# Kernel tuning notes

Measured on AMD Instinct MI355X. Metric: run time of the kernel, lower is better.

The kernel has to match this reference:

```python
import jax, jax.numpy as jnp
import numpy as np

D_MODEL = 1024
D_STATE = 32
EXPAND = 2
D_INNER = D_MODEL * EXPAND
B_SZ = 2
SEQ = 512


def setup_inputs() -> dict:
    key = jax.random.key(0)
    ks = jax.random.split(key, 10)
    x = jax.random.normal(ks[0], (B_SZ, SEQ, D_MODEL), dtype=jnp.float32)
    W_in = jax.random.normal(ks[1], (2 * D_INNER, D_MODEL), dtype=jnp.float32) * 0.02
    A_log = jax.random.uniform(ks[2], (D_INNER, D_STATE), minval=-4.0, maxval=-1.0, dtype=jnp.float32)
    W_B = jax.random.normal(ks[3], (D_STATE, D_MODEL), dtype=jnp.float32) * 0.02
    W_C = jax.random.normal(ks[4], (D_STATE, D_MODEL), dtype=jnp.float32) * 0.02
    W_dt = jax.random.normal(ks[5], (D_INNER, D_MODEL), dtype=jnp.float32) * 0.02
    b_dt = jnp.zeros((D_INNER,), dtype=jnp.float32)
    dt_bias = jnp.zeros((D_INNER,), dtype=jnp.float32) - 4.0
    rope_freq = jax.random.normal(ks[6], (D_STATE // 2,), dtype=jnp.float32) * 0.01
    ln_w = jnp.ones((D_INNER,), dtype=jnp.float32)
    ln_b = jnp.zeros((D_INNER,), dtype=jnp.float32)
    W_out = jax.random.normal(ks[7], (D_MODEL, D_INNER), dtype=jnp.float32) * 0.02
    return {"x": x, "W_in": W_in, "A_log": A_log, "W_B": W_B, "W_C": W_C,
            "W_dt": W_dt, "b_dt": b_dt, "dt_bias": dt_bias, "rope_freq": rope_freq,
            "ln_w": ln_w, "ln_b": ln_b, "W_out": W_out}


def _forward(x, W_in, A_log, W_B, W_C, W_dt, b_dt, dt_bias, rope_freq, ln_w, ln_b, W_out):
    B, L, _ = x.shape
    half = D_STATE // 2
    offset = 0

    xz = jnp.einsum('bld,ed->ble', x, W_in)                 # [B,L,2*D_INNER]
    x_inner = xz[..., :D_INNER]                             # [B,L,DI]
    z = jax.nn.silu(xz[..., D_INNER:])                      # [B,L,DI]

    A = -jnp.exp(A_log)                                     # [DI,DS]
    Bm = jnp.einsum('bld,nd->bln', x, W_B)                  # [B,L,DS]
    Cm = jnp.einsum('bld,nd->bln', x, W_C)                  # [B,L,DS]
    dt = jax.nn.softplus(jnp.einsum('bld,ed->ble', x, W_dt) + b_dt + dt_bias)  # [B,L,DI]

    # trapezoidal discretization
    dtA = dt[..., None] * A                                 # [B,L,DI,DS]
    denom = 1.0 - dtA / 2.0
    A_bar = (1.0 + dtA / 2.0) / denom                       # [B,L,DI,DS]
    B_bar = dt[..., None] / denom                           # [B,L,DI,DS]

    # per-step rope rotation angles: angle_t = rope_freq * (t + offset)
    t_idx = jnp.arange(L, dtype=jnp.float32) + offset       # [L]
    ang = t_idx[:, None] * rope_freq                        # [L,half]
    cos_a = jnp.cos(ang)
    sin_a = jnp.sin(ang)

    def step(state, inp):
        A_t, Bb_t, B_t, x_t, C_t, c_t, s_t = inp
        # state update: [B,DI,DS]
        state = A_t * state + Bb_t * B_t[:, None, :] * x_t[:, :, None]
        real = state[..., :half]
        imag = state[..., half:]
        state = jnp.concatenate([real * c_t - imag * s_t,
                                 real * s_t + imag * c_t], axis=-1)
        y_t = jnp.einsum('bds,bs->bd', state, C_t)          # [B,DI]
        return state, y_t

    state0 = jnp.zeros((B, D_INNER, D_STATE), dtype=x.dtype)
    xs = (jnp.swapaxes(A_bar, 0, 1), jnp.swapaxes(B_bar, 0, 1),
          jnp.swapaxes(Bm, 0, 1), jnp.swapaxes(x_inner, 0, 1),
          jnp.swapaxes(Cm, 0, 1), cos_a, sin_a)
    final_state, ys = jax.lax.scan(step, state0, xs)        # ys: [L,B,DI]
    out = jnp.swapaxes(ys, 0, 1) * z                        # [B,L,DI]

    # LayerNorm over last dim (eps=1e-5, torch default)
    mu = jnp.mean(out, axis=-1, keepdims=True)
    var = jnp.mean((out - mu) ** 2, axis=-1, keepdims=True)
    out = (out - mu) * jax.lax.rsqrt(var + 1e-5) * ln_w + ln_b

    out = jnp.einsum('ble,de->bld', out, W_out)             # [B,L,D_MODEL]
    return out, final_state


def reference(x, W_in, A_log, W_B, W_C, W_dt, b_dt, dt_bias, rope_freq, ln_w, ln_b, W_out):
    return _forward(x, W_in, A_log, W_B, W_C, W_dt, b_dt, dt_bias, rope_freq, ln_w, ln_b, W_out)
```

## Files before the change

### kernel.cpp

```cpp
#include <hip/hip_runtime.h>
#include <math.h>

#define B_SZ 2
#define SEQ 512
#define DM 1024
#define DI 2048
#define DS 32
#define TOK (B_SZ*SEQ)
#define NCH 8
#define CLEN (SEQ/NCH)
#define NPAIRH 32768

#define NFUSED 6272

typedef float v2f __attribute__((ext_vector_type(2)));

__device__ __forceinline__ unsigned short f2bf(float f) {
  unsigned int u = __builtin_bit_cast(unsigned int, f);
  unsigned int r = u + 0x7fffu + ((u >> 16) & 1u);
  return (unsigned short)(r >> 16);
}

template<int CTRL>
__device__ __forceinline__ float row_ror_add(float x) {
  int s = __builtin_amdgcn_update_dpp(0, __builtin_bit_cast(int, x), CTRL, 0xf, 0xf, false);
  return x + __builtin_bit_cast(float, s);
}
__device__ __forceinline__ float row16_sum(float v) {
  v = row_ror_add<0x121>(v);
  v = row_ror_add<0x122>(v);
  v = row_ror_add<0x124>(v);
  v = row_ror_add<0x128>(v);
  return v;
}

__global__ __launch_bounds__(256) void fused_cast(const float* __restrict__ x,
                                                  const float* __restrict__ W_in,
                                                  const float* __restrict__ W_dt,
                                                  const float* __restrict__ W_B,
                                                  const float* __restrict__ W_C,
                                                  const float* __restrict__ W_out,
                                                  unsigned short* __restrict__ xb,
                                                  unsigned short* __restrict__ wcat,
                                                  unsigned short* __restrict__ wob) {
  int g = blockIdx.x * 256 + threadIdx.x;
  const float* s; unsigned short* dd; int off;
  if      (g <  131072) { s = x;     dd = xb;             off = 0; }
  else if (g <  655360) { s = W_in;  dd = wcat;           off = 131072; }
  else if (g <  917504) { s = W_dt;  dd = wcat + 4194304; off = 655360; }
  else if (g <  921600) { s = W_B;   dd = wcat + 6291456; off = 917504; }
  else if (g <  925696) { s = W_C;   dd = wcat + 6324224; off = 921600; }
  else if (g < 1187840) { s = W_out; dd = wob;            off = 925696; }
  else return;
  int i = g - off;
  float4 a = ((const float4*)s)[i * 2];
  float4 b = ((const float4*)s)[i * 2 + 1];
  union { unsigned short us[8]; uint4 v; } o;
  o.us[0] = f2bf(a.x); o.us[1] = f2bf(a.y); o.us[2] = f2bf(a.z); o.us[3] = f2bf(a.w);
  o.us[4] = f2bf(b.x); o.us[5] = f2bf(b.y); o.us[6] = f2bf(b.z); o.us[7] = f2bf(b.w);
  ((uint4*)dd)[i] = o.v;
}

typedef __attribute__((ext_vector_type(8))) short  frag8;
typedef __attribute__((ext_vector_type(4))) float  facc4;

__device__ __forceinline__ void gload_lds16(const unsigned short* g, unsigned short* l) {
  __builtin_amdgcn_global_load_lds((const __attribute__((address_space(1))) unsigned int*)g,
                                   (__attribute__((address_space(3))) unsigned int*)l, 16, 0, 0);
}
__device__ __forceinline__ void gload_lds16f(const float* g, float* l) {
  __builtin_amdgcn_global_load_lds((const __attribute__((address_space(1))) unsigned int*)g,
                                   (__attribute__((address_space(3))) unsigned int*)l, 16, 0, 0);
}

__device__ __forceinline__ float softplus_fast(float v) {
  return fmaxf(v, 0.f) + __logf(1.f + __expf(-fabsf(v)));
}

template<int BMt, int BNt, int MT, bool ROUTE>
__global__ __launch_bounds__(256) void gemm_mfma(const unsigned short* __restrict__ A,
                                                 const unsigned short* __restrict__ Bw,
                                                 int K,
                                                 float* __restrict__ o_xs,
                                                 float* __restrict__ o_zb,
                                                 float* __restrict__ o_dts,
                                                 float* __restrict__ o_bcb,
                                                 const float* __restrict__ b_dt,
                                                 const float* __restrict__ dt_bias,
                                                 float* __restrict__ o_c, int ldc) {
  constexpr int FM = BMt / 32, FN = BNt / 32;
  constexpr int IA = BMt / 64, IB = BNt / 64;
  __shared__ __align__(16) unsigned short As[BMt * 32];
  __shared__ __align__(16) unsigned short Bs[BNt * 32];
  const int tid = threadIdx.x;
  const int w = tid >> 6, lane = tid & 63;
  const int wm = w >> 1, wn = w & 1;
  const int bid = blockIdx.x;
  const int Wk = (bid & 7) * ((int)gridDim.x >> 3) + (bid >> 3);
  const int m0 = (Wk % MT) * BMt;
  const int n0 = (Wk / MT) * BNt;
  const int r = lane & 15, q = lane >> 4;
  const int grow = lane >> 2, gk = (lane & 3) * 8;
  facc4 acc[FM][FN] = {};
  const unsigned short* Ag = A + (size_t)m0 * K + gk;
  const unsigned short* Bg = Bw + (size_t)n0 * K + gk;

  for (int k0 = 0; k0 < K; k0 += 32) {
#pragma unroll
    for (int i = 0; i < IA; ++i) {
      int ch = i * 4 + w;
      gload_lds16(Ag + (size_t)(ch * 16 + grow) * K + k0, &As[ch * 512]);
    }
#pragma unroll
    for (int i = 0; i < IB; ++i) {
      int ch = i * 4 + w;
      gload_lds16(Bg + (size_t)(ch * 16 + grow) * K + k0, &Bs[ch * 512]);
    }
    __syncthreads();
    frag8 af[FM], bf[FN];
#pragma unroll
    for (int i = 0; i < FM; ++i)
      af[i] = *(const frag8*)&As[(wm * (BMt / 2) + i * 16 + r) * 32 + q * 8];
#pragma unroll
    for (int jj = 0; jj < FN; ++jj)
      bf[jj] = *(const frag8*)&Bs[(wn * (BNt / 2) + jj * 16 + r) * 32 + q * 8];
#pragma unroll
    for (int i = 0; i < FM; ++i)
#pragma unroll
      for (int jj = 0; jj < FN; ++jj)
        acc[i][jj] = __builtin_amdgcn_mfma_f32_16x16x32_bf16(af[i], bf[jj], acc[i][jj], 0, 0, 0);
    __syncthreads();
  }

#pragma unroll
  for (int i = 0; i < FM; ++i) {
#pragma unroll
    for (int jj = 0; jj < FN; ++jj) {
      int n = n0 + wn * (BNt / 2) + jj * 16 + r;
      int mb = m0 + wm * (BMt / 2) + i * 16 + q * 4;
      if (ROUTE) {
        if (n < 2048) {
#pragma unroll
          for (int rg = 0; rg < 4; ++rg)
            o_xs[(size_t)(mb + rg) * DI + n] = acc[i][jj][rg];
        } else if (n < 4096) {
#pragma unroll
          for (int rg = 0; rg < 4; ++rg)
            o_zb[(size_t)(mb + rg) * DI + (n - 2048)] = acc[i][jj][rg];
        } else if (n < 6144) {
          int d = n - 4096;
          float bias = b_dt[d] + dt_bias[d];
#pragma unroll
          for (int rg = 0; rg < 4; ++rg)
            o_dts[(size_t)(mb + rg) * DI + d] = softplus_fast(acc[i][jj][rg] + bias);
        } else if (n < 6176) {
#pragma unroll
          for (int rg = 0; rg < 4; ++rg)
            o_bcb[(size_t)(mb + rg) * DS + (n - 6144)] = acc[i][jj][rg];
        } else if (n < 6208) {
#pragma unroll
          for (int rg = 0; rg < 4; ++rg)
            o_bcb[(size_t)TOK * DS + (size_t)(mb + rg) * DS + (n - 6176)] = acc[i][jj][rg];
        }
      } else {
#pragma unroll
        for (int rg = 0; rg < 4; ++rg)
          o_c[(size_t)(mb + rg) * ldc + n] = acc[i][jj][rg];
      }
    }
  }
}


__global__ __launch_bounds__(256) void scan_p1(const float* __restrict__ xs,
                                               const float* __restrict__ dts,
                                               const float* __restrict__ bcb,
                                               const float* __restrict__ A_log,
                                               const float* __restrict__ rope,
                                               float* __restrict__ Pbuf) {
  __shared__ __align__(16) float lds[6144];
  const int blk = blockIdx.x;
  const int c = blk >> 7;
  const int sub = blk & 127;
  const int b = sub >> 6;
  const int dbase = (sub & 63) << 5;
  const int tid = threadIdx.x;
  const int wv = tid >> 6, lane = tid & 63;
  const int j = tid & 15;
  const int ca = (tid >> 4) & 15;
  const int l0 = c * CLEN;
  const size_t base = (size_t)(b * SEQ + l0);

  {
    int row = wv * 16 + (lane >> 3);
    int col = (lane & 7) << 2;
#pragma unroll
    for (int k = 0; k < 2; ++k) {
      gload_lds16f(xs  + (base + row + k * 8) * DI + dbase + col, &lds[(wv * 16 + k * 8) * 32]);
      gload_lds16f(dts + (base + row + k * 8) * DI + dbase + col, &lds[2048 + (wv * 16 + k * 8) * 32]);
    }
#pragma unroll
    for (int k = 0; k < 2; ++k) {
      int seg = wv * 2 + k;
      gload_lds16f(bcb + base * DS + seg * 256 + lane * 4, &lds[4096 + seg * 256]);
    }
  }

  const int dA = dbase + 2 * ca;
  v2f Ar, Ai;
  Ar.x = -0.5f * expf(A_log[dA * DS + j]);
  Ar.y = -0.5f * expf(A_log[(dA + 1) * DS + j]);
  Ai.x = -0.5f * expf(A_log[dA * DS + j + 16]);
  Ai.y = -0.5f * expf(A_log[(dA + 1) * DS + j + 16]);
  const float fr = rope[j];
  float sn, cs, sF, cF;
  sincosf((float)l0 * fr, &sn, &cs);
  sincosf(fr, &sF, &cF);
  __syncthreads();

  v2f p00 = {1.f, 1.f}, p01 = {0.f, 0.f}, p10 = {0.f, 0.f}, p11 = {1.f, 1.f};
  v2f ur = {0.f, 0.f}, ui = {0.f, 0.f};

#pragma unroll 4
  for (int tt = 0; tt < CLEN; ++tt) {
    const int ro = tt * 32;
    v2f xin = *(const v2f*)&lds[ro + 2 * ca];
    v2f dtd = *(const v2f*)&lds[2048 + ro + 2 * ca];
    float Br = lds[4096 + ro + j];
    float Bi = lds[4096 + ro + j + 16];
    v2f hr = dtd * Ar, hi = dtd * Ai;
    v2f invr, invi;
    invr.x = __builtin_amdgcn_rcpf(1.f - hr.x);
    invr.y = __builtin_amdgcn_rcpf(1.f - hr.y);
    invi.x = __builtin_amdgcn_rcpf(1.f - hi.x);
    invi.y = __builtin_amdgcn_rcpf(1.f - hi.y);
    v2f Abr = 2.f * invr - 1.f;
    v2f Abi = 2.f * invi - 1.f;
    v2f dx = dtd * xin;
    v2f bxr = dx * invr * Br;
    v2f bxi = dx * invi * Bi;
    v2f tr = Abr * ur + bxr;
    v2f ti = Abi * ui + bxi;
    ur = tr * cs - ti * sn;
    ui = tr * sn + ti * cs;
    v2f q00 = Abr * p00, q01 = Abr * p01;
    v2f q10 = Abi * p10, q11 = Abi * p11;
    p00 = q00 * cs - q10 * sn; p10 = q00 * sn + q10 * cs;
    p01 = q01 * cs - q11 * sn; p11 = q01 * sn + q11 * cs;
    float nc = fmaf(cs, cF, -sn * sF);
    float ns = fmaf(sn, cF,  cs * sF);
    cs = nc; sn = ns;
  }
  const int pc = (b * 1024 + (dbase >> 1) + ca) * 16 + j;
  float2* Pb2 = (float2*)Pbuf;
  Pb2[(c * 6 + 0) * NPAIRH + pc] = make_float2(p00.x, p00.y);
  Pb2[(c * 6 + 1) * NPAIRH + pc] = make_float2(p01.x, p01.y);
  Pb2[(c * 6 + 2) * NPAIRH + pc] = make_float2(p10.x, p10.y);
  Pb2[(c * 6 + 3) * NPAIRH + pc] = make_float2(p11.x, p11.y);
  Pb2[(c * 6 + 4) * NPAIRH + pc] = make_float2(ur.x, ur.y);
  Pb2[(c * 6 + 5) * NPAIRH + pc] = make_float2(ui.x, ui.y);
}

__global__ __launch_bounds__(256) void scan_p3(const float* __restrict__ xs,
                                               const float* __restrict__ dts,
                                               const float* __restrict__ bcb,
                                               const float* __restrict__ A_log,
                                               const float* __restrict__ rope,
                                               const float* __restrict__ Pbuf,
                                               float* __restrict__ y,
                                               float* __restrict__ fstate) {
  __shared__ __align__(16) float lds[8192];
  const int blk = blockIdx.x;
  const int c = blk >> 7;
  const int sub = blk & 127;
  const int b = sub >> 6;
  const int dbase = (sub & 63) << 5;
  const int tid = threadIdx.x;
  const int wv = tid >> 6, lane = tid & 63;
  const int j = tid & 15;
  const int ca = (tid >> 4) & 15;
  const int l0 = c * CLEN;
  const size_t base = (size_t)(b * SEQ + l0);

  {
    int row = wv * 16 + (lane >> 3);
    int col = (lane & 7) << 2;
#pragma unroll
    for (int k = 0; k < 2; ++k) {
      gload_lds16f(xs  + (base + row + k * 8) * DI + dbase + col, &lds[(wv * 16 + k * 8) * 32]);
      gload_lds16f(dts + (base + row + k * 8) * DI + dbase + col, &lds[2048 + (wv * 16 + k * 8) * 32]);
    }
#pragma unroll
    for (int k = 0; k < 2; ++k) {
      int seg = wv * 2 + k;
      gload_lds16f(bcb + base * DS + seg * 256 + lane * 4, &lds[4096 + seg * 256]);
      gload_lds16f(bcb + (size_t)TOK * DS + base * DS + seg * 256 + lane * 4, &lds[6144 + seg * 256]);
    }
  }

  const int dA = dbase + 2 * ca;
  v2f Ar, Ai;
  Ar.x = -0.5f * expf(A_log[dA * DS + j]);
  Ar.y = -0.5f * expf(A_log[(dA + 1) * DS + j]);
  Ai.x = -0.5f * expf(A_log[dA * DS + j + 16]);
  Ai.y = -0.5f * expf(A_log[(dA + 1) * DS + j + 16]);
  const float fr = rope[j];
  float sn, cs, sF, cF;
  sincosf((float)l0 * fr, &sn, &cs);
  sincosf(fr, &sF, &cF);

  const int pc = (b * 1024 + (dbase >> 1) + ca) * 16 + j;
  const float2* Pb2 = (const float2*)Pbuf;
  v2f sr = {0.f, 0.f}, si = {0.f, 0.f};
  for (int k = 0; k < c; ++k) {
    float2 f;
    f = Pb2[(k * 6 + 0) * NPAIRH + pc]; v2f p00 = {f.x, f.y};
    f = Pb2[(k * 6 + 1) * NPAIRH + pc]; v2f p01 = {f.x, f.y};
    f = Pb2[(k * 6 + 2) * NPAIRH + pc]; v2f p10 = {f.x, f.y};
    f = Pb2[(k * 6 + 3) * NPAIRH + pc]; v2f p11 = {f.x, f.y};
    f = Pb2[(k * 6 + 4) * NPAIRH + pc]; v2f ur  = {f.x, f.y};
    f = Pb2[(k * 6 + 5) * NPAIRH + pc]; v2f ui  = {f.x, f.y};
    v2f nr = p00 * sr + p01 * si + ur;
    v2f ni = p10 * sr + p11 * si + ui;
    sr = nr; si = ni;
  }
  __syncthreads();

  float* yp = y + base * DI + dA;

#pragma unroll 4
  for (int tt = 0; tt < CLEN; ++tt) {
    const int ro = tt * 32;
    v2f xin = *(const v2f*)&lds[ro + 2 * ca];
    v2f dtd = *(const v2f*)&lds[2048 + ro + 2 * ca];
    float Br = lds[4096 + ro + j];
    float Bi = lds[4096 + ro + j + 16];
    float Cr = lds[6144 + ro + j];
    float Ci = lds[6144 + ro + j + 16];
    v2f hr = dtd * Ar, hi = dtd * Ai;
    v2f invr, invi;
    invr.x = __builtin_amdgcn_rcpf(1.f - hr.x);
    invr.y = __builtin_amdgcn_rcpf(1.f - hr.y);
    invi.x = __builtin_amdgcn_rcpf(1.f - hi.x);
    invi.y = __builtin_amdgcn_rcpf(1.f - hi.y);
    v2f Abr = 2.f * invr - 1.f;
    v2f Abi = 2.f * invi - 1.f;
    v2f dx = dtd * xin;
    v2f bxr = dx * invr * Br;
    v2f bxi = dx * invi * Bi;
    v2f tr = Abr * sr + bxr;
    v2f ti = Abi * si + bxi;
    sr = tr * cs - ti * sn;
    si = tr * sn + ti * cs;
    v2f p = sr * Cr + si * Ci;
    float pA = row16_sum(p.x);
    float pB = row16_sum(p.y);
    if (j == 0) *(float2*)&yp[tt * DI] = make_float2(pA, pB);
    float nc = fmaf(cs, cF, -sn * sF);
    float ns = fmaf(sn, cF,  cs * sF);
    cs = nc; sn = ns;
  }
  if (c == NCH - 1) {
    fstate[((size_t)b * DI + dA) * DS + j]          = sr.x;
    fstate[((size_t)b * DI + dA) * DS + j + 16]     = si.x;
    fstate[((size_t)b * DI + dA + 1) * DS + j]      = sr.y;
    fstate[((size_t)b * DI + dA + 1) * DS + j + 16] = si.y;
  }
}

__global__ __launch_bounds__(256) void gate_ln(const float* __restrict__ y,
                                               const float* __restrict__ zb,
                                               const float* __restrict__ lw,
                                               const float* __restrict__ lb,
                                               unsigned short* __restrict__ o) {
  int tok = blockIdx.x;
  int t = threadIdx.x;
  float g[8];
  float sum = 0.f, sq = 0.f;
#pragma unroll
  for (int i = 0; i < 8; ++i) {
    int dd = t + i * 256;
    float yv = y[(size_t)tok * DI + dd];
    float zv = zb[(size_t)tok * DI + dd];
    float sg = zv / (1.f + __expf(-zv));
    float v = yv * sg;
    g[i] = v; sum += v; sq += v * v;
  }
#pragma unroll
  for (int off = 32; off; off >>= 1) { sum += __shfl_xor(sum, off); sq += __shfl_xor(sq, off); }
  __shared__ float rs[4], rq[4];
  int w = t >> 6;
  if ((t & 63) == 0) { rs[w] = sum; rq[w] = sq; }
  __syncthreads();
  sum = rs[0] + rs[1] + rs[2] + rs[3];
  sq  = rq[0] + rq[1] + rq[2] + rq[3];
  float mu = sum * (1.f / DI);
  float var = sq * (1.f / DI) - mu * mu;
  float rstd = rsqrtf(var + 1e-5f);
#pragma unroll
  for (int i = 0; i < 8; ++i) {
    int dd = t + i * 256;
    o[(size_t)tok * DI + dd] = f2bf((g[i] - mu) * rstd * lw[dd] + lb[dd]);
  }
}

extern "C" void kernel_launch(void* const* d_in, const int* in_sizes, int n_in,
                              void* d_out, int out_size, void* d_ws, size_t ws_size,
                              hipStream_t stream) {
  const float* x       = (const float*)d_in[0];
  const float* W_in    = (const float*)d_in[1];
  const float* A_log   = (const float*)d_in[2];
  const float* W_B     = (const float*)d_in[3];
  const float* W_C     = (const float*)d_in[4];
  const float* W_dt    = (const float*)d_in[5];
  const float* b_dt    = (const float*)d_in[6];
  const float* dt_bias = (const float*)d_in[7];
  const float* rope    = (const float*)d_in[8];
  const float* ln_w    = (const float*)d_in[9];
  const float* ln_b    = (const float*)d_in[10];
  const float* W_out   = (const float*)d_in[11];
  float* out = (float*)d_out;
  float* ws = (float*)d_ws;

  float* xs   = ws;
  float* zb   = ws + 2097152;
  float* dts  = ws + 4194304;
  float* bcb  = ws + 6291456;
  unsigned short* wob  = (unsigned short*)(ws + 6356992);
  unsigned short* xb   = (unsigned short*)(ws + 7405568);
  unsigned short* wcat = (unsigned short*)(ws + 7929856);
  float* Pbuf = ws + 7929856;
  float* yb   = ws + 11141120;
  unsigned short* lnb = (unsigned short*)(ws + 13238272);
  float* fstate = out + (size_t)TOK * DM;

  fused_cast<<<4640, 256, 0, stream>>>(x, W_in, W_dt, W_B, W_C, W_out, xb, wcat, wob);
  gemm_mfma<64, 64, 16, true><<<(NFUSED / 64) * (TOK / 64), 256, 0, stream>>>(
      xb, wcat, DM, xs, zb, dts, bcb, b_dt, dt_bias, nullptr, 0);
  scan_p1<<<(NCH - 1) * 128, 256, 0, stream>>>(xs, dts, bcb, A_log, rope, Pbuf);
  scan_p3<<<NCH * 128, 256, 0, stream>>>(xs, dts, bcb, A_log, rope, Pbuf, yb, fstate);
  gate_ln<<<TOK, 256, 0, stream>>>(yb, zb, ln_w, ln_b, lnb);
  gemm_mfma<64, 64, 16, false><<<(DM / 64) * (TOK / 64), 256, 0, stream>>>(
      lnb, wob, DI, nullptr, nullptr, nullptr, nullptr, nullptr, nullptr, out, DM);
}
```

Before: 218.9 us.

## Use BK=64 GEMM tiles and split-K the output projection with a reduction pass

The MFMA GEMM now loads 64-wide K slices per iteration, which halves the number of barrier pairs per tile. The output projection (K=2048) is split into two K halves across twice as many blocks. Each half writes a partial result to workspace, and a new elementwise kernel sums the two partials into the output. This targets low occupancy in the 256-block output GEMM, at the cost of an extra kernel launch and extra partial-buffer traffic.

Result: no change. 215.9 us (-1.4%).

```diff
diff --git a/kernel.cpp b/kernel.cpp
--- a/kernel.cpp
+++ b/kernel.cpp
@@ -77,7 +77,7 @@
   return fmaxf(v, 0.f) + __logf(1.f + __expf(-fabsf(v)));
 }
 
-template<int BMt, int BNt, int MT, bool ROUTE>
+template<int MT, int NT, int KSP, bool ROUTE>
 __global__ __launch_bounds__(256) void gemm_mfma(const unsigned short* __restrict__ A,
                                                  const unsigned short* __restrict__ Bw,
                                                  int K,
@@ -88,56 +88,57 @@
                                                  const float* __restrict__ b_dt,
                                                  const float* __restrict__ dt_bias,
                                                  float* __restrict__ o_c, int ldc) {
-  constexpr int FM = BMt / 32, FN = BNt / 32;
-  constexpr int IA = BMt / 64, IB = BNt / 64;
-  __shared__ __align__(16) unsigned short As[BMt * 32];
-  __shared__ __align__(16) unsigned short Bs[BNt * 32];
+  __shared__ __align__(16) unsigned short As[64 * 64];
+  __shared__ __align__(16) unsigned short Bs[64 * 64];
   const int tid = threadIdx.x;
   const int w = tid >> 6, lane = tid & 63;
   const int wm = w >> 1, wn = w & 1;
   const int bid = blockIdx.x;
   const int Wk = (bid & 7) * ((int)gridDim.x >> 3) + (bid >> 3);
-  const int m0 = (Wk % MT) * BMt;
-  const int n0 = (Wk / MT) * BNt;
+  const int ks = Wk / (MT * NT);
+  const int rem = Wk % (MT * NT);
+  const int m0 = (rem % MT) * 64;
+  const int n0 = (rem / MT) * 64;
+  const int kLen = K / KSP, kBeg = ks * kLen;
   const int r = lane & 15, q = lane >> 4;
-  const int grow = lane >> 2, gk = (lane & 3) * 8;
-  facc4 acc[FM][FN] = {};
-  const unsigned short* Ag = A + (size_t)m0 * K + gk;
-  const unsigned short* Bg = Bw + (size_t)n0 * K + gk;
-
-  for (int k0 = 0; k0 < K; k0 += 32) {
-#pragma unroll
-    for (int i = 0; i < IA; ++i) {
-      int ch = i * 4 + w;
-      gload_lds16(Ag + (size_t)(ch * 16 + grow) * K + k0, &As[ch * 512]);
-    }
-#pragma unroll
-    for (int i = 0; i < IB; ++i) {
-      int ch = i * 4 + w;
-      gload_lds16(Bg + (size_t)(ch * 16 + grow) * K + k0, &Bs[ch * 512]);
+  const int srow = lane >> 3;
+  const int scol = (lane & 7) * 8;
+  facc4 acc[2][2] = {};
+  const unsigned short* Ag = A + (size_t)m0 * K + kBeg;
+  const unsigned short* Bg = Bw + (size_t)n0 * K + kBeg;
+
+  for (int k0 = 0; k0 < kLen; k0 += 64) {
+#pragma unroll
+    for (int k = 0; k < 2; ++k) {
+      int ch = w * 2 + k;
+      gload_lds16(Ag + (size_t)(ch * 8 + srow) * K + k0 + scol, &As[ch * 512]);
+      gload_lds16(Bg + (size_t)(ch * 8 + srow) * K + k0 + scol, &Bs[ch * 512]);
     }
     __syncthreads();
-    frag8 af[FM], bf[FN];
-#pragma unroll
-    for (int i = 0; i < FM; ++i)
-      af[i] = *(const frag8*)&As[(wm * (BMt / 2) + i * 16 + r) * 32 + q * 8];
-#pragma unroll
-    for (int jj = 0; jj < FN; ++jj)
-      bf[jj] = *(const frag8*)&Bs[(wn * (BNt / 2) + jj * 16 + r) * 32 + q * 8];
-#pragma unroll
-    for (int i = 0; i < FM; ++i)
-#pragma unroll
-      for (int jj = 0; jj < FN; ++jj)
-        acc[i][jj] = __builtin_amdgcn_mfma_f32_16x16x32_bf16(af[i], bf[jj], acc[i][jj], 0, 0, 0);
+#pragma unroll
+    for (int kk = 0; kk < 2; ++kk) {
+      frag8 af[2], bf[2];
+#pragma unroll
+      for (int i = 0; i < 2; ++i)
+        af[i] = *(const frag8*)&As[(wm * 32 + i * 16 + r) * 64 + kk * 32 + q * 8];
+#pragma unroll
+      for (int jj = 0; jj < 2; ++jj)
+        bf[jj] = *(const frag8*)&Bs[(wn * 32 + jj * 16 + r) * 64 + kk * 32 + q * 8];
+#pragma unroll
+      for (int i = 0; i < 2; ++i)
+#pragma unroll
+        for (int jj = 0; jj < 2; ++jj)
+          acc[i][jj] = __builtin_amdgcn_mfma_f32_16x16x32_bf16(af[i], bf[jj], acc[i][jj], 0, 0, 0);
+    }
     __syncthreads();
   }
 
 #pragma unroll
-  for (int i = 0; i < FM; ++i) {
-#pragma unroll
-    for (int jj = 0; jj < FN; ++jj) {
-      int n = n0 + wn * (BNt / 2) + jj * 16 + r;
-      int mb = m0 + wm * (BMt / 2) + i * 16 + q * 4;
+  for (int i = 0; i < 2; ++i) {
+#pragma unroll
+    for (int jj = 0; jj < 2; ++jj) {
+      int n = n0 + wn * 32 + jj * 16 + r;
+      int mb = m0 + wm * 32 + i * 16 + q * 4;
       if (ROUTE) {
         if (n < 2048) {
 #pragma unroll
@@ -163,14 +164,23 @@
             o_bcb[(size_t)TOK * DS + (size_t)(mb + rg) * DS + (n - 6176)] = acc[i][jj][rg];
         }
       } else {
+        float* oc = o_c + (size_t)ks * (MT * 64) * ldc;
 #pragma unroll
         for (int rg = 0; rg < 4; ++rg)
-          o_c[(size_t)(mb + rg) * ldc + n] = acc[i][jj][rg];
+          oc[(size_t)(mb + rg) * ldc + n] = acc[i][jj][rg];
       }
     }
   }
 }
 
+__global__ __launch_bounds__(256) void addk(const float* __restrict__ p0,
+                                            const float* __restrict__ p1,
+                                            float* __restrict__ o) {
+  int i = blockIdx.x * 256 + threadIdx.x;
+  float4 a = ((const float4*)p0)[i];
+  float4 b = ((const float4*)p1)[i];
+  ((float4*)o)[i] = make_float4(a.x + b.x, a.y + b.y, a.z + b.z, a.w + b.w);
+}
 
 __global__ __launch_bounds__(256) void scan_p1(const float* __restrict__ xs,
                                                const float* __restrict__ dts,
@@ -432,14 +442,16 @@
   float* Pbuf = ws + 7929856;
   float* yb   = ws + 11141120;
   unsigned short* lnb = (unsigned short*)(ws + 13238272);
+  float* Pk   = ws;
   float* fstate = out + (size_t)TOK * DM;
 
   fused_cast<<<4640, 256, 0, stream>>>(x, W_in, W_dt, W_B, W_C, W_out, xb, wcat, wob);
-  gemm_mfma<64, 64, 16, true><<<(NFUSED / 64) * (TOK / 64), 256, 0, stream>>>(
+  gemm_mfma<16, 98, 1, true><<<16 * 98, 256, 0, stream>>>(
       xb, wcat, DM, xs, zb, dts, bcb, b_dt, dt_bias, nullptr, 0);
   scan_p1<<<(NCH - 1) * 128, 256, 0, stream>>>(xs, dts, bcb, A_log, rope, Pbuf);
   scan_p3<<<NCH * 128, 256, 0, stream>>>(xs, dts, bcb, A_log, rope, Pbuf, yb, fstate);
   gate_ln<<<TOK, 256, 0, stream>>>(yb, zb, ln_w, ln_b, lnb);
-  gemm_mfma<64, 64, 16, false><<<(DM / 64) * (TOK / 64), 256, 0, stream>>>(
-      lnb, wob, DI, nullptr, nullptr, nullptr, nullptr, nullptr, nullptr, out, DM);
-}
+  gemm_mfma<16, 16, 2, false><<<16 * 16 * 2, 256, 0, stream>>>(
+      lnb, wob, DI, nullptr, nullptr, nullptr, nullptr, nullptr, nullptr, Pk, DM);
+  addk<<<(TOK * DM) / 1024, 256, 0, stream>>>(Pk, Pk + (size_t)TOK * DM, out);
+}
```
